# Kernel optimization log

Hardware: AMD Instinct MI355X
Metric: run time of the kernel (lower is better)

The kernel has to match this reference:

```python
import jax, jax.numpy as jnp
import numpy as np

F = 4        # number of factors
M = 256      # codebook size per factor
D = 8192     # hypervector dimension
B = 256      # batch of composite vectors to factorize
ITERS = 10   # resonator iterations


def setup_inputs() -> dict:
    key = jax.random.key(0)
    k1, k2 = jax.random.split(key, 2)
    # bipolar (+1/-1) codebooks, shape [F, M, D]
    cb = jnp.sign(jax.random.normal(k1, (F, M, D), dtype=jnp.float32))
    codebooks = jnp.where(cb == 0, 1.0, cb)
    # composite inputs: bind (elementwise product) of one random codevector per factor
    idx = jax.random.randint(k2, (B, F), 0, M)                       # [B, F]
    chosen = codebooks[jnp.arange(F)[None, :], idx]                  # [B, F, D]
    inp = jnp.prod(chosen, axis=1)                                   # [B, D]
    return {"input": inp, "codebooks": codebooks}


def _stage_concurrent(inp, est, codebooks):
    # est: [B, F, D]; codebooks: [F, M, D]; inp: [B, D]
    n = est.shape[1]
    # inv_others[:, f] = prod_{j != f} est[:, j]  (bipolar inverse == identity)
    inv_others = jnp.stack(
        [jnp.prod(jnp.concatenate([est[:, :f], est[:, f + 1:]], axis=1), axis=1)
         for f in range(n)], axis=1)                                  # [B, F, D]
    new_est = inp[:, None, :] * inv_others                            # bind -> [B, F, D]
    sim = jnp.einsum('bfd,fmd->bfm', new_est, codebooks)              # similarity
    # activation == 'NONE'
    out = jnp.einsum('bfm,fmd->bfd', sim, codebooks)                  # dot_similarity
    return jnp.sign(out)


def reference(input, codebooks):
    Bn = input.shape[0]
    # init estimates = multiset (sum) of each codebook, broadcast over batch
    init = jnp.broadcast_to(jnp.sum(codebooks, axis=1)[None], (Bn, F, D)).astype(input.dtype)

    def cond(state):
        _, k, done = state
        return jnp.logical_and(k < ITERS, jnp.logical_not(done))

    def body(state):
        est, k, _ = state
        new = _stage_concurrent(input, est, codebooks)
        return (new, k + 1, jnp.all(new == est))

    est, k, _ = jax.lax.while_loop(cond, body, (init, jnp.int32(0), jnp.array(False)))
    # cleanup: nearest codevector per factor (argmax similarity)
    sim = jnp.einsum('bfd,fmd->bfm', est, codebooks)
    outcome = jnp.argmax(sim, axis=-1)                                # [B, F] indices
    return outcome, k
```

## Files before the change

### kernel.cpp

```cpp
#include <hip/hip_runtime.h>

#define B_SZ 256
#define F_SZ 4
#define M_SZ 256
#define D_SZ 8192
#define NITER 10

typedef signed char i8;
typedef unsigned long long u64;
typedef signed char c16 __attribute__((ext_vector_type(16)));
typedef int v4i __attribute__((ext_vector_type(4)));

#define NBFM (B_SZ * F_SZ * M_SZ)

#define OFF_CB    ((size_t)0)
#define OFF_CBT   ((size_t)8  << 20)
#define OFF_IN8   ((size_t)16 << 20)
#define OFF_CBBT  ((size_t)18 << 20)
#define OFF_INB   ((size_t)19 << 20)
#define OFF_ESB0  ((size_t)20 << 20)
#define OFF_EZB0  ((size_t)21 << 20)
#define OFF_ESB1  ((size_t)22 << 20)
#define OFF_EZB1  ((size_t)23 << 20)
#define OFF_SIMX  ((size_t)24 << 20)
#define OFF_SIMI  ((size_t)25 << 20)
#define OFF_P1    ((size_t)26 << 20)
#define OFF_S32   ((size_t)42 << 20)
#define OFF_PDIG  (OFF_S32 + (size_t)F_SZ * D_SZ * 4)
#define OFF_CHG   (OFF_PDIG + (size_t)4 * F_SZ * D_SZ)


__global__ __launch_bounds__(256) void k_cvt_cb(const float* __restrict__ src,
                                                i8* __restrict__ cb, i8* __restrict__ cbt) {
  __shared__ i8 tile[32][33];
  const int bid = blockIdx.x;
  const int f = bid >> 11;
  const int rem = bid & 2047;
  const int m0 = (rem >> 8) << 5;
  const int d0 = (rem & 255) << 5;
  const int t = threadIdx.x;
  const int i = t >> 3, j = (t & 7) << 2;
  const float4 v = *(const float4*)(src + ((size_t)(f * M_SZ + m0 + i)) * D_SZ + d0 + j);
  char4 c;
  c.x = v.x > 0.f ? 1 : -1;
  c.y = v.y > 0.f ? 1 : -1;
  c.z = v.z > 0.f ? 1 : -1;
  c.w = v.w > 0.f ? 1 : -1;
  *(char4*)(cb + ((size_t)(f * M_SZ + m0 + i)) * D_SZ + d0 + j) = c;
  tile[i][j + 0] = c.x; tile[i][j + 1] = c.y; tile[i][j + 2] = c.z; tile[i][j + 3] = c.w;
  __syncthreads();
  const int dd = t >> 3, jm = (t & 7) << 2;
  char4 o;
  o.x = tile[jm + 0][dd]; o.y = tile[jm + 1][dd]; o.z = tile[jm + 2][dd]; o.w = tile[jm + 3][dd];
  *(char4*)(cbt + ((size_t)(f * D_SZ + d0 + dd)) * M_SZ + m0 + jm) = o;
}

__global__ __launch_bounds__(256) void k_cvt_in(const float* __restrict__ src, i8* __restrict__ dst) {
  const int idx = blockIdx.x * 256 + threadIdx.x;
  const float4 v = ((const float4*)src)[idx];
  char4 c;
  c.x = v.x > 0.f ? 1 : -1;
  c.y = v.y > 0.f ? 1 : -1;
  c.z = v.z > 0.f ? 1 : -1;
  c.w = v.w > 0.f ? 1 : -1;
  ((char4*)dst)[idx] = c;
}

__global__ __launch_bounds__(256) void k_pack_cb(const i8* __restrict__ cb, u64* __restrict__ cbbT) {
  const int id = blockIdx.x * 256 + threadIdx.x;
  const int f = id >> 15;
  const int rem = id & 32767;
  const int w = rem >> 8;
  const int m = rem & 255;
  const i8* src = cb + ((size_t)(f * M_SZ + m)) * D_SZ + w * 64;
  u64 r = 0;
  #pragma unroll
  for (int k = 0; k < 4; ++k) {
    c16 v = *(const c16*)(src + k * 16);
    u64 part = 0;
    #pragma unroll
    for (int j = 0; j < 16; ++j) part |= ((u64)(((unsigned char)v[j]) >> 7)) << j;
    r |= part << (k * 16);
  }
  cbbT[((size_t)(f * 128 + w)) * 256 + m] = r;
}

__global__ __launch_bounds__(256) void k_pack_in(const i8* __restrict__ in8, u64* __restrict__ inb) {
  const int id = blockIdx.x * 256 + threadIdx.x;
  const int b = id >> 7;
  const int w = id & 127;
  const i8* src = in8 + (size_t)b * D_SZ + w * 64;
  u64 r = 0;
  #pragma unroll
  for (int k = 0; k < 4; ++k) {
    c16 v = *(const c16*)(src + k * 16);
    u64 part = 0;
    #pragma unroll
    for (int j = 0; j < 16; ++j) part |= ((u64)(((unsigned char)v[j]) >> 7)) << j;
    r |= part << (k * 16);
  }
  inb[(size_t)b * 128 + w] = r;
}

__global__ __launch_bounds__(256) void k_S(const i8* __restrict__ cb, int* __restrict__ S) {
  const int id = blockIdx.x * 256 + threadIdx.x;
  const int f = id >> 13, d = id & 8191;
  const i8* p = cb + (size_t)f * M_SZ * D_SZ + d;
  int s = 0;
  for (int m = 0; m < M_SZ; ++m) s += p[(size_t)m * D_SZ];
  S[id] = s;
}

__global__ __launch_bounds__(256) void k_P(const int* __restrict__ S, i8* __restrict__ pdig) {
  const int d = blockIdx.x * 256 + threadIdx.x;
  const int s0 = S[d], s1 = S[D_SZ + d], s2 = S[2 * D_SZ + d], s3 = S[3 * D_SZ + d];
  int P[4];
  P[0] = s1 * s2 * s3;
  P[1] = s0 * s2 * s3;
  P[2] = s0 * s1 * s3;
  P[3] = s0 * s1 * s2;
  for (int f = 0; f < 4; ++f) {
    int x = P[f];
    #pragma unroll
    for (int p = 0; p < 3; ++p) {
      int r = (x + 64) >> 7;
      int dg = x - (r << 7);
      pdig[((size_t)(p * F_SZ + f)) * D_SZ + d] = (i8)dg;
      x = r;
    }
    pdig[((size_t)(3 * F_SZ + f)) * D_SZ + d] = (i8)x;
  }
}


__global__ __launch_bounds__(256) void ga2_kernel(
    const i8* __restrict__ in8, const i8* __restrict__ cb,
    const i8* __restrict__ pdig, int* __restrict__ p1)
{
  __shared__ __align__(16) i8 lA[64 * 48];
  __shared__ __align__(16) i8 lB[128 * 48];

  const int bid = blockIdx.x;
  const int s = bid & 3;
  const int p = (bid >> 2) & 3;
  const int f = (bid >> 4) & 3;
  const int ct = bid >> 6;
  const int b0 = (ct >> 1) * 64;
  const int m0 = (ct & 1) * 128;
  const int ksteps = 64;
  const int kbase = s << 11;

  const int t = threadIdx.x;
  const int lane = t & 63;
  const int wv = t >> 6;
  const int wrow = (wv >> 1) * 32;
  const int wcol = (wv & 1) * 64;

  const int arow = t >> 1;
  const int aoff = (t & 1) * 16;
  const i8* pB  = cb   + ((size_t)(f * M_SZ + m0 + arow)) * D_SZ + aoff;
  const i8* pDg = pdig + ((size_t)(p * F_SZ + f)) * D_SZ + aoff;
  const i8* pIn = in8  + (size_t)(b0 + arow) * D_SZ + aoff;

  v4i acc[2][4];
  #pragma unroll
  for (int tr = 0; tr < 2; ++tr)
    #pragma unroll
    for (int tc = 0; tc < 4; ++tc) acc[tr][tc] = 0;

  c16 va = 0, vb = 0;
  {
    const int kk = kbase;
    vb = (*(const c16*)(pB + kk)) * (*(const c16*)(pDg + kk));
    if (t < 128) va = *(const c16*)(pIn + kk);
  }

  for (int j = 0; j < ksteps; ++j) {
    c16 sa = va, sb = vb;
    if (j + 1 < ksteps) {
      const int kk = kbase + (j + 1) * 32;
      vb = (*(const c16*)(pB + kk)) * (*(const c16*)(pDg + kk));
      if (t < 128) va = *(const c16*)(pIn + kk);
    }
    __syncthreads();
    if (t < 128) *(c16*)&lA[arow * 48 + aoff] = sa;
    *(c16*)&lB[arow * 48 + aoff] = sb;
    __syncthreads();

    const int rsel = lane & 15;
    const int kq = (lane >> 4) * 8;
    long af[2], bf[4];
    #pragma unroll
    for (int tr = 0; tr < 2; ++tr) af[tr] = *(const long*)&lA[(wrow + tr * 16 + rsel) * 48 + kq];
    #pragma unroll
    for (int tc = 0; tc < 4; ++tc) bf[tc] = *(const long*)&lB[(wcol + tc * 16 + rsel) * 48 + kq];
    #pragma unroll
    for (int tr = 0; tr < 2; ++tr)
      #pragma unroll
      for (int tc = 0; tc < 4; ++tc)
        acc[tr][tc] = __builtin_amdgcn_mfma_i32_16x16x32_i8(af[tr], bf[tc], acc[tr][tc], 0, 0, 0);
  }

  const int colb = lane & 15;
  const int rowq = (lane >> 4) * 4;
  const size_t obase = (size_t)(p * 4 + s) * NBFM;
  #pragma unroll
  for (int tr = 0; tr < 2; ++tr)
    #pragma unroll
    for (int tc = 0; tc < 4; ++tc)
      #pragma unroll
      for (int r = 0; r < 4; ++r) {
        const int b = b0 + wrow + tr * 16 + rowq + r;
        const int m = m0 + wcol + tc * 16 + colb;
        p1[obase + (((size_t)(b * F_SZ + f)) << 8) + m] = acc[tr][tc][r];
      }
}

__global__ __launch_bounds__(256) void k_digits1(const int* __restrict__ p1, i8* __restrict__ simx) {
  const int idx = blockIdx.x * 256 + threadIdx.x;
  long long sim = 0;
  #pragma unroll
  for (int p = 3; p >= 0; --p) {
    long long g = 0;
    #pragma unroll
    for (int s = 0; s < 4; ++s) g += (long long)p1[(size_t)(p * 4 + s) * NBFM + idx];
    sim = sim * 128 + g;
  }
  int x = (int)sim;
  const int r1 = (x + 128) >> 8;
  const int d0 = x - (r1 << 8);
  const int r2 = (r1 + 128) >> 8;
  const int d1 = r1 - (r2 << 8);
  const size_t bf = (size_t)(idx >> 8);
  const int m = idx & 255;
  simx[bf * 768 + m] = (i8)d0;
  simx[bf * 768 + 256 + m] = (i8)d1;
  simx[bf * 768 + 512 + m] = (i8)r2;
}


template<int MODE>
__global__ __launch_bounds__(256) void ga_bit(
    const u64* __restrict__ esb, const u64* __restrict__ ezb,
    const u64* __restrict__ inb, const u64* __restrict__ cbbT,
    i8* __restrict__ simx, int* __restrict__ sim_int)
{
  __shared__ u64 AL[128][4];
  __shared__ int C0[2];

  const int bid = blockIdx.x;
  const int f = bid & 3;
  const int b0 = (bid >> 2) * 2;
  const int t = threadIdx.x;
  if (t < 2) C0[t] = 0;
  __syncthreads();

  {
    const int r = t >> 7, w = t & 127;
    const int b = b0 + r;
    u64 s, nz;
    if (MODE == 0) {
      int ffs[3]; int c = 0;
      for (int ff = 0; ff < 4; ++ff) if (ff != f) ffs[c++] = ff;
      const size_t base = (size_t)b * 4 * 128;
      s = inb[(size_t)b * 128 + w]
        ^ esb[base + ffs[0] * 128 + w] ^ esb[base + ffs[1] * 128 + w] ^ esb[base + ffs[2] * 128 + w];
      nz = ~(ezb[base + ffs[0] * 128 + w] | ezb[base + ffs[1] * 128 + w] | ezb[base + ffs[2] * 128 + w]);
    } else {
      const size_t a = ((size_t)b * 4 + f) * 128 + w;
      s = esb[a];
      nz = ~ezb[a];
    }
    AL[w][r * 2] = s;
    AL[w][r * 2 + 1] = nz;
    atomicAdd(&C0[r], __popcll(nz));
  }
  __syncthreads();

  const int m = t;
  int a0 = 0, a1 = 0;
  const u64* pc = cbbT + (size_t)f * 128 * 256 + m;
  for (int w = 0; w < 128; ++w) {
    const u64 cbw = pc[w * 256];
    const u64 s0 = AL[w][0], z0 = AL[w][1], s1 = AL[w][2], z1 = AL[w][3];
    a0 += (int)__popcll((s0 ^ cbw) & z0);
    a1 += (int)__popcll((s1 ^ cbw) & z1);
  }
  const int sim0 = C0[0] - 2 * a0;
  const int sim1 = C0[1] - 2 * a1;

  if (MODE == 0) {
    int d1 = (sim0 + 128) >> 8; int d0v = sim0 - (d1 << 8);
    const size_t bf0 = ((size_t)b0 * 4 + f) * 768;
    simx[bf0 + m] = (i8)d0v; simx[bf0 + 256 + m] = (i8)d1;
    d1 = (sim1 + 128) >> 8; d0v = sim1 - (d1 << 8);
    const size_t bf1 = ((size_t)(b0 + 1) * 4 + f) * 768;
    simx[bf1 + m] = (i8)d0v; simx[bf1 + 256 + m] = (i8)d1;
  } else {
    sim_int[((size_t)b0 * 4 + f) * 256 + m] = sim0;
    sim_int[((size_t)(b0 + 1) * 4 + f) * 256 + m] = sim1;
  }
}


template<int NP, bool FIRST>
__global__ __launch_bounds__(256) void gb_kernel(
    const i8* __restrict__ simx, const i8* __restrict__ cbt,
    const u64* __restrict__ esp, const u64* __restrict__ ezp,
    const int* __restrict__ S32,
    u64* __restrict__ esn, u64* __restrict__ ezn,
    int* __restrict__ changed, int it)
{
  __shared__ __align__(16) i8 lB[8 * 8 * 64 * 8];
  __shared__ int chgf;

  const int bid = blockIdx.x;
  const int f = bid & 3;
  const int ct = bid >> 2;
  const int b0 = (ct >> 6) * 64;
  const int d0 = (ct & 63) * 128;

  const int t = threadIdx.x;
  if (t == 0) chgf = 0;
  const int lane = t & 63;
  const int wv = t >> 6;
  const int wrow = (wv >> 1) * 32;
  const int wcol = (wv & 1) * 64;

  {
    const int c = t & 15;
    const int dr0 = t >> 4;
    const int ks = c >> 1;
    const int q0 = (c & 1) * 2;
    #pragma unroll
    for (int i = 0; i < 8; ++i) {
      const int dr = dr0 + i * 16;
      union { c16 v; u64 u[2]; } x;
      x.v = *(const c16*)(cbt + ((size_t)(f * D_SZ + d0 + dr)) * M_SZ + c * 16);
      const int tile = dr >> 4;
      const int col = dr & 15;
      *(u64*)&lB[((((ks * 8 + tile) * 4 + q0) * 16 + col)) * 8] = x.u[0];
      *(u64*)&lB[((((ks * 8 + tile) * 4 + q0 + 1) * 16 + col)) * 8] = x.u[1];
    }
  }
  __syncthreads();

  v4i acc[NP][2][4];
  #pragma unroll
  for (int pp = 0; pp < NP; ++pp)
    #pragma unroll
    for (int tr = 0; tr < 2; ++tr)
      #pragma unroll
      for (int tc = 0; tc < 4; ++tc) acc[pp][tr][tc] = 0;

  const int rsel = lane & 15;
  const int kq = (lane >> 4) * 8;
  const int tb = wcol >> 4;

  #pragma unroll
  for (int ks = 0; ks < 8; ++ks) {
    long bf[4];
    #pragma unroll
    for (int tc = 0; tc < 4; ++tc)
      bf[tc] = *(const long*)&lB[((ks * 8 + tb + tc) * 64 + lane) * 8];
    #pragma unroll
    for (int pp = 0; pp < NP; ++pp) {
      long af[2];
      #pragma unroll
      for (int tr = 0; tr < 2; ++tr) {
        const int row = b0 + wrow + tr * 16 + rsel;
        af[tr] = *(const long*)(simx + ((size_t)(row * 4 + f)) * 768 + pp * 256 + ks * 32 + kq);
      }
      #pragma unroll
      for (int tr = 0; tr < 2; ++tr)
        #pragma unroll
        for (int tc = 0; tc < 4; ++tc)
          acc[pp][tr][tc] = __builtin_amdgcn_mfma_i32_16x16x32_i8(af[tr], bf[tc], acc[pp][tr][tc], 0, 0, 0);
    }
  }

  bool chl = false;
  const int colb = lane & 15;

  #pragma unroll
  for (int tr = 0; tr < 2; ++tr) {
    unsigned long long bs[4][4], bz[4][4];
    #pragma unroll
    for (int r = 0; r < 4; ++r)
      #pragma unroll
      for (int tc = 0; tc < 4; ++tc) {
        int o = acc[0][tr][tc][r];
        if (NP > 1) o += acc[1][tr][tc][r] * 256;
        if (NP > 2) o += acc[2][tr][tc][r] * 65536;
        bs[r][tc] = __ballot(o < 0);
        bz[r][tc] = __ballot(o == 0);
        if (FIRST) {
          const int sg = (o > 0) - (o < 0);
          const int d = d0 + wcol + tc * 16 + colb;
          chl |= (sg != S32[f * D_SZ + d]);
        }
      }
    u64 ws = 0, wz = 0;
    #pragma unroll
    for (int rl = 0; rl < 16; ++rl) {
      const int g = rl >> 2, r = rl & 3;
      u64 vs = 0, vz = 0;
      #pragma unroll
      for (int tc = 0; tc < 4; ++tc) {
        vs |= ((bs[r][tc] >> (g * 16)) & 0xFFFFull) << (tc * 16);
        vz |= ((bz[r][tc] >> (g * 16)) & 0xFFFFull) << (tc * 16);
      }
      if (lane == rl) { ws = vs; wz = vz; }
    }
    if (lane < 16) {
      const int row = b0 + wrow + tr * 16 + lane;
      const size_t wi = ((size_t)(row * 4 + f)) * 128 + ((d0 + wcol) >> 6);
      if (!FIRST) chl |= (ws != esp[wi]) | (wz != ezp[wi]);
      esn[wi] = ws;
      ezn[wi] = wz;
    }
  }
  if (chl) atomicOr(&chgf, 1);
  __syncthreads();
  if (t == 0 && chgf) atomicOr(&changed[it], 1);
}


__global__ __launch_bounds__(256) void k_argmax(const int* __restrict__ sim_int,
                                                const int* __restrict__ chg,
                                                int* __restrict__ out) {
  __shared__ long long red[256];
  const int bf = blockIdx.x;
  const int m = threadIdx.x;
  const int sim = sim_int[(size_t)bf * 256 + m];
  red[m] = ((long long)sim << 32) | (long long)(unsigned)(255 - m);
  __syncthreads();
  for (int s = 128; s > 0; s >>= 1) {
    if (m < s) { if (red[m + s] > red[m]) red[m] = red[m + s]; }
    __syncthreads();
  }
  if (m == 0) {
    out[bf] = 255 - (int)(red[0] & 0xFFFF);
    if (bf == 0) {
      int k = NITER;
      for (int i = 1; i <= NITER; ++i) if (chg[i] == 0) { k = i; break; }
      out[B_SZ * F_SZ] = k;
    }
  }
}


extern "C" void kernel_launch(void* const* d_in, const int* in_sizes, int n_in,
                              void* d_out, int out_size, void* d_ws, size_t ws_size,
                              hipStream_t stream) {
  const float* f_in = (const float*)d_in[0];
  const float* f_cb = (const float*)d_in[1];
  int* out = (int*)d_out;
  char* ws = (char*)d_ws;

  i8*  cb8  = (i8*)(ws + OFF_CB);
  i8*  cbt8 = (i8*)(ws + OFF_CBT);
  i8*  in8  = (i8*)(ws + OFF_IN8);
  u64* cbbT = (u64*)(ws + OFF_CBBT);
  u64* inb  = (u64*)(ws + OFF_INB);
  u64* esb0 = (u64*)(ws + OFF_ESB0);
  u64* ezb0 = (u64*)(ws + OFF_EZB0);
  u64* esb1 = (u64*)(ws + OFF_ESB1);
  u64* ezb1 = (u64*)(ws + OFF_EZB1);
  i8*  simx = (i8*)(ws + OFF_SIMX);
  int* simI = (int*)(ws + OFF_SIMI);
  int* p1   = (int*)(ws + OFF_P1);
  int* S32  = (int*)(ws + OFF_S32);
  i8*  pdig = (i8*)(ws + OFF_PDIG);
  int* chg  = (int*)(ws + OFF_CHG);

  hipMemsetAsync(chg, 0, 64, stream);
  k_cvt_cb<<<dim3(8192), dim3(256), 0, stream>>>(f_cb, cb8, cbt8);
  k_cvt_in<<<dim3(2048), dim3(256), 0, stream>>>(f_in, in8);
  k_pack_cb<<<dim3(512), dim3(256), 0, stream>>>(cb8, cbbT);
  k_pack_in<<<dim3(128), dim3(256), 0, stream>>>(in8, inb);
  k_S<<<dim3(128), dim3(256), 0, stream>>>(cb8, S32);
  k_P<<<dim3(32), dim3(256), 0, stream>>>(S32, pdig);

  ga2_kernel<<<dim3(512), dim3(256), 0, stream>>>(in8, cb8, pdig, p1);
  k_digits1<<<dim3(1024), dim3(256), 0, stream>>>(p1, simx);
  gb_kernel<3, true><<<dim3(1024), dim3(256), 0, stream>>>(
      simx, cbt8, nullptr, nullptr, S32, esb0, ezb0, chg, 1);

  u64* cs = esb0; u64* cz = ezb0; u64* ns = esb1; u64* nz = ezb1;
  for (int it = 2; it <= NITER; ++it) {
    ga_bit<0><<<dim3(512), dim3(256), 0, stream>>>(cs, cz, inb, cbbT, simx, nullptr);
    gb_kernel<2, false><<<dim3(1024), dim3(256), 0, stream>>>(
        simx, cbt8, cs, cz, nullptr, ns, nz, chg, it);
    u64* ts = cs; cs = ns; ns = ts;
    u64* tz = cz; cz = nz; nz = tz;
  }

  ga_bit<1><<<dim3(512), dim3(256), 0, stream>>>(cs, cz, inb, cbbT, nullptr, simI);
  k_argmax<<<dim3(1024), dim3(256), 0, stream>>>(simI, chg, out);
}
```

Baseline: 592.1 us.

## Skip converged iterations, use base-255 digits, fuse final similarity with argmax

Iteration kernels now check the convergence flag from the previous step and return early, so the remaining work after convergence drops to a cheap launch. The first-iteration similarity GEMM switches from four base-128 digit planes with 4 K-splits to three base-255 planes with 8 K-splits, which gives more blocks and fewer total planes. The final similarity and argmax are fused into one kernel, and the estimate buffers are updated in place instead of double-buffered. Popcount accumulation now uses a wavefront shuffle reduction instead of per-thread shared atomics. In-place updates rely on ga_bit finishing before gb_kernel runs, and the >>3 scaling assumes the products are divisible by 8.

```diff
diff --git a/kernel.cpp b/kernel.cpp
--- a/kernel.cpp
+++ b/kernel.cpp
@@ -18,16 +18,13 @@
 #define OFF_IN8   ((size_t)16 << 20)
 #define OFF_CBBT  ((size_t)18 << 20)
 #define OFF_INB   ((size_t)19 << 20)
-#define OFF_ESB0  ((size_t)20 << 20)
-#define OFF_EZB0  ((size_t)21 << 20)
-#define OFF_ESB1  ((size_t)22 << 20)
-#define OFF_EZB1  ((size_t)23 << 20)
-#define OFF_SIMX  ((size_t)24 << 20)
-#define OFF_SIMI  ((size_t)25 << 20)
-#define OFF_P1    ((size_t)26 << 20)
-#define OFF_S32   ((size_t)42 << 20)
+#define OFF_ESB   ((size_t)20 << 20)
+#define OFF_EZB   ((size_t)21 << 20)
+#define OFF_SIMX  ((size_t)22 << 20)
+#define OFF_P1    ((size_t)23 << 20)
+#define OFF_S32   ((size_t)48 << 20)
 #define OFF_PDIG  (OFF_S32 + (size_t)F_SZ * D_SZ * 4)
-#define OFF_CHG   (OFF_PDIG + (size_t)4 * F_SZ * D_SZ)
+#define OFF_CHG   (OFF_PDIG + (size_t)3 * F_SZ * D_SZ)
 
 
 __global__ __launch_bounds__(256) void k_cvt_cb(const float* __restrict__ src,
@@ -120,15 +117,16 @@
   P[2] = s0 * s1 * s3;
   P[3] = s0 * s1 * s2;
   for (int f = 0; f < 4; ++f) {
-    int x = P[f];
-    #pragma unroll
-    for (int p = 0; p < 3; ++p) {
-      int r = (x + 64) >> 7;
-      int dg = x - (r << 7);
+    int x = P[f] >> 3;
+    #pragma unroll
+    for (int p = 0; p < 2; ++p) {
+      const int y = x + 127;
+      const int q = (y >= 0) ? (y / 255) : -((-y + 254) / 255);
+      const int dg = x - q * 255;
       pdig[((size_t)(p * F_SZ + f)) * D_SZ + d] = (i8)dg;
-      x = r;
-    }
-    pdig[((size_t)(3 * F_SZ + f)) * D_SZ + d] = (i8)x;
+      x = q;
+    }
+    pdig[((size_t)(2 * F_SZ + f)) * D_SZ + d] = (i8)x;
   }
 }
 
@@ -141,14 +139,16 @@
   __shared__ __align__(16) i8 lB[128 * 48];
 
   const int bid = blockIdx.x;
-  const int s = bid & 3;
-  const int p = (bid >> 2) & 3;
-  const int f = (bid >> 4) & 3;
-  const int ct = bid >> 6;
+  const int s = bid & 7;
+  const int r = bid >> 3;
+  const int p = r % 3;
+  const int q = r / 3;
+  const int f = q & 3;
+  const int ct = q >> 2;
   const int b0 = (ct >> 1) * 64;
   const int m0 = (ct & 1) * 128;
-  const int ksteps = 64;
-  const int kbase = s << 11;
+  const int ksteps = 32;
+  const int kbase = s << 10;
 
   const int t = threadIdx.x;
   const int lane = t & 63;
@@ -203,29 +203,30 @@
 
   const int colb = lane & 15;
   const int rowq = (lane >> 4) * 4;
-  const size_t obase = (size_t)(p * 4 + s) * NBFM;
+  const size_t obase = (size_t)(p * 8 + s) * NBFM;
   #pragma unroll
   for (int tr = 0; tr < 2; ++tr)
     #pragma unroll
     for (int tc = 0; tc < 4; ++tc)
       #pragma unroll
-      for (int r = 0; r < 4; ++r) {
-        const int b = b0 + wrow + tr * 16 + rowq + r;
+      for (int rr = 0; rr < 4; ++rr) {
+        const int b = b0 + wrow + tr * 16 + rowq + rr;
         const int m = m0 + wcol + tc * 16 + colb;
-        p1[obase + (((size_t)(b * F_SZ + f)) << 8) + m] = acc[tr][tc][r];
+        p1[obase + (((size_t)(b * F_SZ + f)) << 8) + m] = acc[tr][tc][rr];
       }
 }
 
 __global__ __launch_bounds__(256) void k_digits1(const int* __restrict__ p1, i8* __restrict__ simx) {
   const int idx = blockIdx.x * 256 + threadIdx.x;
-  long long sim = 0;
-  #pragma unroll
-  for (int p = 3; p >= 0; --p) {
-    long long g = 0;
-    #pragma unroll
-    for (int s = 0; s < 4; ++s) g += (long long)p1[(size_t)(p * 4 + s) * NBFM + idx];
-    sim = sim * 128 + g;
-  }
+  long long g[3];
+  #pragma unroll
+  for (int p = 0; p < 3; ++p) {
+    long long gg = 0;
+    #pragma unroll
+    for (int s = 0; s < 8; ++s) gg += (long long)p1[(size_t)(p * 8 + s) * NBFM + idx];
+    g[p] = gg;
+  }
+  const long long sim = g[0] + 255LL * g[1] + 65025LL * g[2];
   int x = (int)sim;
   const int r1 = (x + 128) >> 8;
   const int d0 = x - (r1 << 8);
@@ -239,14 +240,15 @@
 }
 
 
-template<int MODE>
 __global__ __launch_bounds__(256) void ga_bit(
     const u64* __restrict__ esb, const u64* __restrict__ ezb,
     const u64* __restrict__ inb, const u64* __restrict__ cbbT,
-    i8* __restrict__ simx, int* __restrict__ sim_int)
+    i8* __restrict__ simx, const int* __restrict__ changed, int it)
 {
   __shared__ u64 AL[128][4];
   __shared__ int C0[2];
+
+  if (changed[it - 1] == 0) return;
 
   const int bid = blockIdx.x;
   const int f = bid & 3;
@@ -258,28 +260,25 @@
   {
     const int r = t >> 7, w = t & 127;
     const int b = b0 + r;
-    u64 s, nz;
-    if (MODE == 0) {
-      int ffs[3]; int c = 0;
-      for (int ff = 0; ff < 4; ++ff) if (ff != f) ffs[c++] = ff;
-      const size_t base = (size_t)b * 4 * 128;
-      s = inb[(size_t)b * 128 + w]
-        ^ esb[base + ffs[0] * 128 + w] ^ esb[base + ffs[1] * 128 + w] ^ esb[base + ffs[2] * 128 + w];
-      nz = ~(ezb[base + ffs[0] * 128 + w] | ezb[base + ffs[1] * 128 + w] | ezb[base + ffs[2] * 128 + w]);
-    } else {
-      const size_t a = ((size_t)b * 4 + f) * 128 + w;
-      s = esb[a];
-      nz = ~ezb[a];
-    }
+    int ffs[3]; int c = 0;
+    for (int ff = 0; ff < 4; ++ff) if (ff != f) ffs[c++] = ff;
+    const size_t base = (size_t)b * 4 * 128;
+    const u64 s = inb[(size_t)b * 128 + w]
+      ^ esb[base + ffs[0] * 128 + w] ^ esb[base + ffs[1] * 128 + w] ^ esb[base + ffs[2] * 128 + w];
+    const u64 nz = ~(ezb[base + ffs[0] * 128 + w] | ezb[base + ffs[1] * 128 + w] | ezb[base + ffs[2] * 128 + w]);
     AL[w][r * 2] = s;
     AL[w][r * 2 + 1] = nz;
-    atomicAdd(&C0[r], __popcll(nz));
+    int pcv = (int)__popcll(nz);
+    #pragma unroll
+    for (int off = 32; off >= 1; off >>= 1) pcv += __shfl_down(pcv, off);
+    if ((t & 63) == 0) atomicAdd(&C0[r], pcv);
   }
   __syncthreads();
 
   const int m = t;
   int a0 = 0, a1 = 0;
   const u64* pc = cbbT + (size_t)f * 128 * 256 + m;
+  #pragma unroll 4
   for (int w = 0; w < 128; ++w) {
     const u64 cbw = pc[w * 256];
     const u64 s0 = AL[w][0], z0 = AL[w][1], s1 = AL[w][2], z1 = AL[w][3];
@@ -289,30 +288,26 @@
   const int sim0 = C0[0] - 2 * a0;
   const int sim1 = C0[1] - 2 * a1;
 
-  if (MODE == 0) {
-    int d1 = (sim0 + 128) >> 8; int d0v = sim0 - (d1 << 8);
-    const size_t bf0 = ((size_t)b0 * 4 + f) * 768;
-    simx[bf0 + m] = (i8)d0v; simx[bf0 + 256 + m] = (i8)d1;
-    d1 = (sim1 + 128) >> 8; d0v = sim1 - (d1 << 8);
-    const size_t bf1 = ((size_t)(b0 + 1) * 4 + f) * 768;
-    simx[bf1 + m] = (i8)d0v; simx[bf1 + 256 + m] = (i8)d1;
-  } else {
-    sim_int[((size_t)b0 * 4 + f) * 256 + m] = sim0;
-    sim_int[((size_t)(b0 + 1) * 4 + f) * 256 + m] = sim1;
-  }
+  int d1 = (sim0 + 128) >> 8; int d0v = sim0 - (d1 << 8);
+  const size_t bf0 = ((size_t)b0 * 4 + f) * 768;
+  simx[bf0 + m] = (i8)d0v; simx[bf0 + 256 + m] = (i8)d1;
+  d1 = (sim1 + 128) >> 8; d0v = sim1 - (d1 << 8);
+  const size_t bf1 = ((size_t)(b0 + 1) * 4 + f) * 768;
+  simx[bf1 + m] = (i8)d0v; simx[bf1 + 256 + m] = (i8)d1;
 }
 
 
 template<int NP, bool FIRST>
 __global__ __launch_bounds__(256) void gb_kernel(
     const i8* __restrict__ simx, const i8* __restrict__ cbt,
-    const u64* __restrict__ esp, const u64* __restrict__ ezp,
+    u64* __restrict__ esb, u64* __restrict__ ezb,
     const int* __restrict__ S32,
-    u64* __restrict__ esn, u64* __restrict__ ezn,
     int* __restrict__ changed, int it)
 {
   __shared__ __align__(16) i8 lB[8 * 8 * 64 * 8];
   __shared__ int chgf;
+
+  if (!FIRST) { if (changed[it - 1] == 0) return; }
 
   const int bid = blockIdx.x;
   const int f = bid & 3;
@@ -386,14 +381,14 @@
   for (int tr = 0; tr < 2; ++tr) {
     unsigned long long bs[4][4], bz[4][4];
     #pragma unroll
-    for (int r = 0; r < 4; ++r)
+    for (int rr = 0; rr < 4; ++rr)
       #pragma unroll
       for (int tc = 0; tc < 4; ++tc) {
-        int o = acc[0][tr][tc][r];
-        if (NP > 1) o += acc[1][tr][tc][r] * 256;
-        if (NP > 2) o += acc[2][tr][tc][r] * 65536;
-        bs[r][tc] = __ballot(o < 0);
-        bz[r][tc] = __ballot(o == 0);
+        int o = acc[0][tr][tc][rr];
+        if (NP > 1) o += acc[1][tr][tc][rr] * 256;
+        if (NP > 2) o += acc[2][tr][tc][rr] * 65536;
+        bs[rr][tc] = __ballot(o < 0);
+        bz[rr][tc] = __ballot(o == 0);
         if (FIRST) {
           const int sg = (o > 0) - (o < 0);
           const int d = d0 + wcol + tc * 16 + colb;
@@ -403,21 +398,21 @@
     u64 ws = 0, wz = 0;
     #pragma unroll
     for (int rl = 0; rl < 16; ++rl) {
-      const int g = rl >> 2, r = rl & 3;
+      const int g = rl >> 2, rr = rl & 3;
       u64 vs = 0, vz = 0;
       #pragma unroll
       for (int tc = 0; tc < 4; ++tc) {
-        vs |= ((bs[r][tc] >> (g * 16)) & 0xFFFFull) << (tc * 16);
-        vz |= ((bz[r][tc] >> (g * 16)) & 0xFFFFull) << (tc * 16);
+        vs |= ((bs[rr][tc] >> (g * 16)) & 0xFFFFull) << (tc * 16);
+        vz |= ((bz[rr][tc] >> (g * 16)) & 0xFFFFull) << (tc * 16);
       }
       if (lane == rl) { ws = vs; wz = vz; }
     }
     if (lane < 16) {
       const int row = b0 + wrow + tr * 16 + lane;
       const size_t wi = ((size_t)(row * 4 + f)) * 128 + ((d0 + wcol) >> 6);
-      if (!FIRST) chl |= (ws != esp[wi]) | (wz != ezp[wi]);
-      esn[wi] = ws;
-      ezn[wi] = wz;
+      if (!FIRST) chl |= (ws != esb[wi]) | (wz != ezb[wi]);
+      esb[wi] = ws;
+      ezb[wi] = wz;
     }
   }
   if (chl) atomicOr(&chgf, 1);
@@ -426,22 +421,64 @@
 }
 
 
-__global__ __launch_bounds__(256) void k_argmax(const int* __restrict__ sim_int,
-                                                const int* __restrict__ chg,
-                                                int* __restrict__ out) {
-  __shared__ long long red[256];
-  const int bf = blockIdx.x;
-  const int m = threadIdx.x;
-  const int sim = sim_int[(size_t)bf * 256 + m];
-  red[m] = ((long long)sim << 32) | (long long)(unsigned)(255 - m);
-  __syncthreads();
-  for (int s = 128; s > 0; s >>= 1) {
-    if (m < s) { if (red[m + s] > red[m]) red[m] = red[m + s]; }
+__global__ __launch_bounds__(256) void k_final(
+    const u64* __restrict__ esb, const u64* __restrict__ ezb,
+    const u64* __restrict__ cbbT, const int* __restrict__ chg,
+    int* __restrict__ out)
+{
+  __shared__ u64 AL[128][4];
+  __shared__ int C0[2];
+  __shared__ long long red0[256], red1[256];
+
+  const int bid = blockIdx.x;
+  const int f = bid & 3;
+  const int b0 = (bid >> 2) * 2;
+  const int t = threadIdx.x;
+  if (t < 2) C0[t] = 0;
+  __syncthreads();
+
+  {
+    const int r = t >> 7, w = t & 127;
+    const int b = b0 + r;
+    const size_t a = ((size_t)b * 4 + f) * 128 + w;
+    const u64 s = esb[a];
+    const u64 nz = ~ezb[a];
+    AL[w][r * 2] = s;
+    AL[w][r * 2 + 1] = nz;
+    int pcv = (int)__popcll(nz);
+    #pragma unroll
+    for (int off = 32; off >= 1; off >>= 1) pcv += __shfl_down(pcv, off);
+    if ((t & 63) == 0) atomicAdd(&C0[r], pcv);
+  }
+  __syncthreads();
+
+  const int m = t;
+  int a0 = 0, a1 = 0;
+  const u64* pc = cbbT + (size_t)f * 128 * 256 + m;
+  #pragma unroll 4
+  for (int w = 0; w < 128; ++w) {
+    const u64 cbw = pc[w * 256];
+    const u64 s0 = AL[w][0], z0 = AL[w][1], s1 = AL[w][2], z1 = AL[w][3];
+    a0 += (int)__popcll((s0 ^ cbw) & z0);
+    a1 += (int)__popcll((s1 ^ cbw) & z1);
+  }
+  const int sim0 = C0[0] - 2 * a0;
+  const int sim1 = C0[1] - 2 * a1;
+
+  red0[m] = ((long long)sim0 << 32) | (long long)(unsigned)(255 - m);
+  red1[m] = ((long long)sim1 << 32) | (long long)(unsigned)(255 - m);
+  __syncthreads();
+  for (int s2 = 128; s2 > 0; s2 >>= 1) {
+    if (m < s2) {
+      if (red0[m + s2] > red0[m]) red0[m] = red0[m + s2];
+      if (red1[m + s2] > red1[m]) red1[m] = red1[m + s2];
+    }
     __syncthreads();
   }
   if (m == 0) {
-    out[bf] = 255 - (int)(red[0] & 0xFFFF);
-    if (bf == 0) {
+    out[b0 * 4 + f] = 255 - (int)(red0[0] & 0xFFFF);
+    out[(b0 + 1) * 4 + f] = 255 - (int)(red1[0] & 0xFFFF);
+    if (bid == 0) {
       int k = NITER;
       for (int i = 1; i <= NITER; ++i) if (chg[i] == 0) { k = i; break; }
       out[B_SZ * F_SZ] = k;
@@ -463,12 +500,9 @@
   i8*  in8  = (i8*)(ws + OFF_IN8);
   u64* cbbT = (u64*)(ws + OFF_CBBT);
   u64* inb  = (u64*)(ws + OFF_INB);
-  u64* esb0 = (u64*)(ws + OFF_ESB0);
-  u64* ezb0 = (u64*)(ws + OFF_EZB0);
-  u64* esb1 = (u64*)(ws + OFF_ESB1);
-  u64* ezb1 = (u64*)(ws + OFF_EZB1);
+  u64* esb  = (u64*)(ws + OFF_ESB);
+  u64* ezb  = (u64*)(ws + OFF_EZB);
   i8*  simx = (i8*)(ws + OFF_SIMX);
-  int* simI = (int*)(ws + OFF_SIMI);
   int* p1   = (int*)(ws + OFF_P1);
   int* S32  = (int*)(ws + OFF_S32);
   i8*  pdig = (i8*)(ws + OFF_PDIG);
@@ -482,20 +516,16 @@
   k_S<<<dim3(128), dim3(256), 0, stream>>>(cb8, S32);
   k_P<<<dim3(32), dim3(256), 0, stream>>>(S32, pdig);
 
-  ga2_kernel<<<dim3(512), dim3(256), 0, stream>>>(in8, cb8, pdig, p1);
+  ga2_kernel<<<dim3(768), dim3(256), 0, stream>>>(in8, cb8, pdig, p1);
   k_digits1<<<dim3(1024), dim3(256), 0, stream>>>(p1, simx);
   gb_kernel<3, true><<<dim3(1024), dim3(256), 0, stream>>>(
-      simx, cbt8, nullptr, nullptr, S32, esb0, ezb0, chg, 1);
-
-  u64* cs = esb0; u64* cz = ezb0; u64* ns = esb1; u64* nz = ezb1;
+      simx, cbt8, esb, ezb, S32, chg, 1);
+
   for (int it = 2; it <= NITER; ++it) {
-    ga_bit<0><<<dim3(512), dim3(256), 0, stream>>>(cs, cz, inb, cbbT, simx, nullptr);
+    ga_bit<<<dim3(512), dim3(256), 0, stream>>>(esb, ezb, inb, cbbT, simx, chg, it);
     gb_kernel<2, false><<<dim3(1024), dim3(256), 0, stream>>>(
-        simx, cbt8, cs, cz, nullptr, ns, nz, chg, it);
-    u64* ts = cs; cs = ns; ns = ts;
-    u64* tz = cz; cz = nz; nz = tz;
-  }
-
-  ga_bit<1><<<dim3(512), dim3(256), 0, stream>>>(cs, cz, inb, cbbT, nullptr, simI);
-  k_argmax<<<dim3(1024), dim3(256), 0, stream>>>(simI, chg, out);
-}
+        simx, cbt8, esb, ezb, nullptr, chg, it);
+  }
+
+  k_final<<<dim3(512), dim3(256), 0, stream>>>(esb, ezb, cbbT, chg, out);
+}
```

Measured after the change: 565.1 us. 4.6% less time.
